# Optimization experiments

Hardware: AMD Instinct MI355X
Metric: run time of the kernel (lower is better)

## Reference

```python
import jax, jax.numpy as jnp
import numpy as np

CHUNK = 400
L = 50          # encoder kernel and stride
JUMP = CHUNK // L  # 8 new frames per streaming step
N = 128         # encoder feature dim
B = 128         # bottleneck dim
H = 512         # TCN hidden dim
K = 3           # depthwise kernel size
R, X = 2, 7     # repeats x blocks, dilations 2^0..2^6
BUF = 516       # ring buffer length: JUMP + 2*sum(dilations)*R = 8 + 508
EPS = 1e-8


def setup_inputs() -> dict:
    key = jax.random.key(0)
    ks = jax.random.split(key, 16)
    nb = R * X
    w = lambda i, shape: jax.random.normal(ks[i], shape, jnp.float32) * 0.05
    return dict(
        mixture=jax.random.normal(ks[0], (1, 2, CHUNK), jnp.float32),
        encoder_buffer=jax.random.uniform(ks[1], (1, N, BUF), dtype=jnp.float32),
        layernorm_buffer=jax.random.normal(ks[2], (1, B, BUF), jnp.float32),
        W_enc=w(3, (N, 2, L)),              # encoder Conv1d(2->N, k=L, s=L)
        ln_g=jnp.ones((N,), jnp.float32),    # channelwise LayerNorm affine
        ln_b=jnp.zeros((N,), jnp.float32),
        W_bn=w(4, (B, N)),                   # bottleneck 1x1 conv
        blk_w1=w(5, (nb, H, B)),             # per-block pointwise in
        blk_p1=jnp.full((nb,), 0.25, jnp.float32),
        blk_g1=jnp.ones((nb, H), jnp.float32),
        blk_b1=jnp.zeros((nb, H), jnp.float32),
        blk_dw=w(6, (nb, H, K)),             # depthwise dilated conv
        blk_p2=jnp.full((nb,), 0.25, jnp.float32),
        blk_g2=jnp.ones((nb, H), jnp.float32),
        blk_b2=jnp.zeros((nb, H), jnp.float32),
        blk_w2=w(7, (nb, B, H)),             # per-block pointwise out
        W_mask=w(8, (N, B)),                 # mask 1x1 conv (C=1 source)
        W_dec=w(9, (L, N)),                  # decoder basis Linear(N->L)
    )


def _cln(x, g, b):
    # channelwise LayerNorm: normalize over channel dim per time frame. x: [1,C,T]
    mu = jnp.mean(x, axis=1, keepdims=True)
    var = jnp.var(x, axis=1, keepdims=True)
    return g[None, :, None] * (x - mu) * jax.lax.rsqrt(var + EPS) + b[None, :, None]


def _prelu(x, a):
    return jnp.where(x >= 0, x, a * x)


def _dwconv(x, w, d):
    # valid dilated depthwise conv. x: [1,H,T], w: [H,K] -> [1,H,T-(K-1)*d]
    return jax.lax.conv_general_dilated(
        x, w[:, None, :], window_strides=(1,), padding='VALID',
        rhs_dilation=(d,), feature_group_count=H,
        dimension_numbers=('NCH', 'OIH', 'NCH'))


def reference(mixture, encoder_buffer, layernorm_buffer, W_enc, ln_g, ln_b, W_bn,
              blk_w1, blk_p1, blk_g1, blk_b1, blk_dw, blk_p2, blk_g2, blk_b2,
              blk_w2, W_mask, W_dec):
    # --- encoder: Conv1d(2->N, k=L, s=L) + ReLU -> JUMP new frames, ring-shift buffer
    enc = jax.nn.relu(jax.lax.conv_general_dilated(
        mixture, W_enc, window_strides=(L,), padding='VALID',
        dimension_numbers=('NCH', 'OIH', 'NCH')))          # [1,N,JUMP]
    encoder_buffer = jnp.concatenate([encoder_buffer[:, :, JUMP:], enc], axis=2)

    # --- separator front-end (network[0:2]): cLN + bottleneck 1x1, per-frame causal
    ln_new = jnp.einsum('oc,bct->bot', W_bn, _cln(enc, ln_g, ln_b))  # [1,B,JUMP]
    layernorm_buffer = jnp.concatenate([layernorm_buffer[:, :, JUMP:], ln_new], axis=2)

    # --- TCN (network[2]): valid causal dilated blocks, each shrinks time by 2*d
    x = layernorm_buffer                                   # [1,B,516]
    for i in range(R * X):
        d = 2 ** (i % X)
        y = jnp.einsum('hc,bct->bht', blk_w1[i], x)
        y = _cln(_prelu(y, blk_p1[i]), blk_g1[i], blk_b1[i])
        y = _dwconv(y, blk_dw[i], d)                       # time -= (K-1)*d
        y = _cln(_prelu(y, blk_p2[i]), blk_g2[i], blk_b2[i])
        y = jnp.einsum('ch,bht->bct', blk_w2[i], y)
        x = x[:, :, (K - 1) * d:] + y                      # residual on trailing frames
    # x: [1,B,JUMP]

    # --- mask conv (network[3]) + ReLU, reshape to [1,C=1,N,JUMP]
    mask = jax.nn.relu(jnp.einsum('nc,bct->bnt', W_mask, x)).reshape(1, 1, N, JUMP)

    # --- decoder: mask the newest JUMP encoder frames, basis Linear(N->L), stride=L
    src_w = encoder_buffer[:, None, :, -JUMP:] * mask      # [1,1,N,JUMP]
    est_source = jnp.einsum('ln,bcnt->bctl', W_dec, src_w).reshape(1, 1, JUMP * L)
    return est_source, encoder_buffer, layernorm_buffer
```

## Files before the change

### kernel.cpp

```cpp
#include <hip/hip_runtime.h>

#define CHUNK 400
#define LWIN 50
#define JUMP 8
#define NCH 128
#define BCH 128
#define HCH 512
#define NBLK 14
#define BUF 516
#define SHIFT 508
#define EPSV 1e-8f
#define NWG 136
#define NGRP 8
#define GSIZE 17

__device__ __forceinline__ void cstore(float* p, float v) {
    __hip_atomic_store(p, v, __ATOMIC_RELAXED, __HIP_MEMORY_SCOPE_AGENT);
}

__device__ __forceinline__ void gsync(unsigned* bar, int slot, int tid, int wg, int doInv) {
    __syncthreads();
    if (tid == 0) {
        unsigned* base = bar + slot * (9 * 32);
        unsigned* loc  = base + (wg & 7) * 32;
        unsigned* root = base + 8 * 32;
        unsigned prev = __hip_atomic_fetch_add(loc, 1u, __ATOMIC_RELAXED,
                                               __HIP_MEMORY_SCOPE_AGENT);
        if (prev == GSIZE - 1)
            __hip_atomic_fetch_add(root, 1u, __ATOMIC_RELAXED,
                                   __HIP_MEMORY_SCOPE_AGENT);
        while (__hip_atomic_load(root, __ATOMIC_RELAXED, __HIP_MEMORY_SCOPE_AGENT) < NGRP)
            __builtin_amdgcn_s_sleep(2);
        if (doInv)
            (void)__hip_atomic_load(root, __ATOMIC_ACQUIRE, __HIP_MEMORY_SCOPE_AGENT);
    }
    __syncthreads();
}

__device__ __forceinline__ void stage1_core(
    int tid, int lane, int wid, int t0, int nf,
    const float* __restrict__ w1b, float aPr,
    const float* __restrict__ gv, const float* __restrict__ bv,
    float* __restrict__ yout, float* redf, float* statsf, const float* xsv)
{
    float acc[4] = {0.f, 0.f, 0.f, 0.f};
    const float4* __restrict__ wr = (const float4*)(w1b + (size_t)tid * BCH);
    const float4* __restrict__ xv = (const float4*)xsv;
    #pragma unroll 4
    for (int c4 = 0; c4 < 32; ++c4) {
        float4 w = wr[c4];
        #pragma unroll
        for (int f = 0; f < 4; ++f) {
            float4 x = xv[f * 32 + c4];
            acc[f] += w.x * x.x + w.y * x.y + w.z * x.z + w.w * x.w;
        }
    }
    #pragma unroll
    for (int f = 0; f < 4; ++f) acc[f] = acc[f] >= 0.f ? acc[f] : aPr * acc[f];
    for (int f = 0; f < nf; ++f) {
        float s = acc[f], q = acc[f] * acc[f];
        #pragma unroll
        for (int o = 32; o; o >>= 1) { s += __shfl_xor(s, o); q += __shfl_xor(q, o); }
        if (lane == 0) { redf[(wid * 4 + f) * 2] = s; redf[(wid * 4 + f) * 2 + 1] = q; }
    }
    __syncthreads();
    if (tid < nf) {
        float s = 0.f, q = 0.f;
        #pragma unroll
        for (int w = 0; w < 8; ++w) { s += redf[(w * 4 + tid) * 2]; q += redf[(w * 4 + tid) * 2 + 1]; }
        float mean = s * (1.f / HCH);
        float var = q * (1.f / HCH) - mean * mean;
        statsf[tid * 2] = mean; statsf[tid * 2 + 1] = rsqrtf(var + EPSV);
    }
    __syncthreads();
    float gg = gv[tid], bb = bv[tid];
    for (int f = 0; f < nf; ++f)
        cstore(&yout[(t0 + f) * HCH + tid],
               gg * (acc[f] - statsf[f * 2]) * statsf[f * 2 + 1] + bb);
}

__global__ __launch_bounds__(512) void k_fused(
    const float* __restrict__ mixture, const float* __restrict__ inEnc,
    const float* __restrict__ inLn, const float* __restrict__ Wenc,
    const float* __restrict__ lng, const float* __restrict__ lnb,
    const float* __restrict__ Wbn, const float* __restrict__ w1,
    const float* __restrict__ p1, const float* __restrict__ g1,
    const float* __restrict__ b1, const float* __restrict__ dwc,
    const float* __restrict__ p2, const float* __restrict__ g2,
    const float* __restrict__ b2, const float* __restrict__ w2,
    const float* __restrict__ Wmask, const float* __restrict__ Wdec,
    float* __restrict__ est, float* __restrict__ outEnc, float* __restrict__ outLn,
    unsigned* __restrict__ bar, float* __restrict__ enc,
    float* __restrict__ xbuf, float* __restrict__ ybuf,
    int nx, int ny, int doInv)
{
    __shared__ float xs[4 * BCH];
    __shared__ float ys[4 * 528];
    __shared__ float redf[8 * 4 * 2];
    __shared__ float statsf[4 * 2];

    const int wg = blockIdx.x;
    const int tid = threadIdx.x;
    const int lane = tid & 63, wid = tid >> 6;

    if (wg < 8) {
        int t = wg;
        float e = 0.f;
        if (tid < 128) {
            int c = tid;
            const float* w = Wenc + c * 100;
            const float* m = mixture + t * LWIN;
            #pragma unroll 10
            for (int l = 0; l < LWIN; ++l) e += m[l] * w[l] + m[CHUNK + l] * w[LWIN + l];
            e = fmaxf(e, 0.f);
            cstore(&enc[t * NCH + c], e);
            outEnc[c * BUF + SHIFT + t] = e;
            float s = e, q = e * e;
            #pragma unroll
            for (int o = 32; o; o >>= 1) { s += __shfl_xor(s, o); q += __shfl_xor(q, o); }
            if (lane == 0) { redf[(wid * 4) * 2] = s; redf[(wid * 4) * 2 + 1] = q; }
        }
        __syncthreads();
        if (tid < 128) {
            float S = redf[0] + redf[8], Q = redf[1] + redf[9];
            float mean = S * (1.f / NCH);
            float var = Q * (1.f / NCH) - mean * mean;
            float r = rsqrtf(var + EPSV);
            xs[tid] = lng[tid] * (e - mean) * r + lnb[tid];
        }
        __syncthreads();
        if (tid < 128) {
            float acc = 0.f;
            const float4* wr = (const float4*)(Wbn + tid * NCH);
            const float4* nv = (const float4*)xs;
            #pragma unroll 8
            for (int j4 = 0; j4 < 32; ++j4) {
                float4 w = wr[j4]; float4 x = nv[j4];
                acc += w.x * x.x + w.y * x.y + w.z * x.z + w.w * x.w;
            }
            outLn[tid * BUF + SHIFT + t] = acc;
            cstore(&xbuf[(SHIFT + t) * BCH + tid], acc);
        }
    } else {
        int ch = wg - 8;
        for (int t = tid; t < SHIFT; t += 512)
            outEnc[ch * BUF + t] = inEnc[ch * BUF + t + JUMP];
        if (ch < 127) {
            int f = tid >> 7, c = tid & 127;
            int t = 4 * ch + f;
            float v = inLn[c * BUF + t + JUMP];
            cstore(&xbuf[t * BCH + c], v);
            outLn[c * BUF + t] = v;
        }
    }
    gsync(bar, 0, tid, wg, doInv);

    {
        int t0 = 4 * wg;
        if (t0 < BUF) {
            int nf = min(4, BUF - t0);
            for (int idx = tid; idx < nf * BCH; idx += 512) xs[idx] = xbuf[t0 * BCH + idx];
            __syncthreads();
            stage1_core(tid, lane, wid, t0, nf, w1, p1[0], g1, b1, ybuf, redf, statsf, xs);
        }
    }
    gsync(bar, 1, tid, wg, doInv);

    const float* xin = xbuf;
    int T = BUF;
    for (int i = 0; i < NBLK; ++i) {
        float* xout = xbuf + (size_t)((i + 1) % nx) * (BUF * BCH);
        const float* ycur = ybuf + (size_t)(i % ny) * (BUF * HCH);
        float* ynext = ybuf + (size_t)((i + 1) % ny) * (BUF * HCH);
        int d = 1 << (i % 7);
        int Tout = T - 2 * d;
        int t0 = 4 * wg;
        if (t0 < Tout) {
            int nf = min(4, Tout - t0);
            const float* dwb = dwc + (size_t)i * HCH * 3;
            float d0 = dwb[tid * 3], d1 = dwb[tid * 3 + 1], d2 = dwb[tid * 3 + 2];
            float a2 = p2[i];
            float y[4];
            for (int f = 0; f < nf; ++f) {
                int t = t0 + f;
                float v = d0 * ycur[t * HCH + tid] + d1 * ycur[(t + d) * HCH + tid]
                        + d2 * ycur[(t + 2 * d) * HCH + tid];
                y[f] = v >= 0.f ? v : a2 * v;
            }
            for (int f = 0; f < nf; ++f) {
                float s = y[f], q = y[f] * y[f];
                #pragma unroll
                for (int o = 32; o; o >>= 1) { s += __shfl_xor(s, o); q += __shfl_xor(q, o); }
                if (lane == 0) { redf[(wid * 4 + f) * 2] = s; redf[(wid * 4 + f) * 2 + 1] = q; }
            }
            __syncthreads();
            if (tid < nf) {
                float s = 0.f, q = 0.f;
                #pragma unroll
                for (int w = 0; w < 8; ++w) { s += redf[(w * 4 + tid) * 2]; q += redf[(w * 4 + tid) * 2 + 1]; }
                float mean = s * (1.f / HCH);
                float var = q * (1.f / HCH) - mean * mean;
                statsf[tid * 2] = mean; statsf[tid * 2 + 1] = rsqrtf(var + EPSV);
            }
            __syncthreads();
            {
                float gg = g2[i * HCH + tid], bb = b2[i * HCH + tid];
                int pidx = (tid >> 7) * 132 + (tid & 127);
                for (int f = 0; f < nf; ++f)
                    ys[f * 528 + pidx] = gg * (y[f] - statsf[f * 2]) * statsf[f * 2 + 1] + bb;
            }
            __syncthreads();
            int c = tid >> 2, p = tid & 3;
            float acc[4] = {0.f, 0.f, 0.f, 0.f};
            const float4* wr = (const float4*)(w2 + (size_t)i * BCH * HCH + c * HCH + p * 128);
            const float* yb = ys + p * 132;
            #pragma unroll 4
            for (int j4 = 0; j4 < 32; ++j4) {
                float4 w = wr[j4];
                #pragma unroll
                for (int f = 0; f < 4; ++f) {
                    float4 x = *(const float4*)&yb[f * 528 + j4 * 4];
                    acc[f] += w.x * x.x + w.y * x.y + w.z * x.z + w.w * x.w;
                }
            }
            for (int f = 0; f < nf; ++f) {
                acc[f] += __shfl_xor(acc[f], 1);
                acc[f] += __shfl_xor(acc[f], 2);
            }
            if (p == 0) {
                for (int f = 0; f < nf; ++f) {
                    int t = t0 + f;
                    float xv = xin[(t + 2 * d) * BCH + c] + acc[f];
                    cstore(&xout[t * BCH + c], xv);
                    xs[f * BCH + c] = xv;
                }
            }
            __syncthreads();
            if (i < NBLK - 1) {
                stage1_core(tid, lane, wid, t0, nf,
                            w1 + (size_t)(i + 1) * HCH * BCH, p1[i + 1],
                            g1 + (i + 1) * HCH, b1 + (i + 1) * HCH, ynext, redf, statsf, xs);
            } else {
                int cc = tid & 127, f = tid >> 7;
                float m = 0.f;
                const float4* wm = (const float4*)(Wmask + cc * BCH);
                const float4* xv = (const float4*)(xs + f * BCH);
                #pragma unroll 8
                for (int j4 = 0; j4 < 32; ++j4) {
                    float4 w = wm[j4]; float4 x = xv[j4];
                    m += w.x * x.x + w.y * x.y + w.z * x.z + w.w * x.w;
                }
                m = fmaxf(m, 0.f);
                ys[f * BCH + cc] = m * enc[(t0 + f) * NCH + cc];
                __syncthreads();
                if (tid < 4 * LWIN) {
                    int ff = tid / LWIN, l = tid % LWIN;
                    float e = 0.f;
                    const float4* wd = (const float4*)(Wdec + l * NCH);
                    const float4* sv = (const float4*)(ys + ff * BCH);
                    #pragma unroll 8
                    for (int j4 = 0; j4 < 32; ++j4) {
                        float4 w = wd[j4]; float4 x = sv[j4];
                        e += w.x * x.x + w.y * x.y + w.z * x.z + w.w * x.w;
                    }
                    est[(t0 + ff) * LWIN + l] = e;
                }
            }
        }
        if (i < NBLK - 1) gsync(bar, 2 + i, tid, wg, doInv);
        T = Tout;
        xin = xout;
    }
}

extern "C" void kernel_launch(void* const* d_in, const int* in_sizes, int n_in,
                              void* d_out, int out_size, void* d_ws, size_t ws_size,
                              hipStream_t stream) {
    const float* mixture = (const float*)d_in[0];
    const float* inEnc   = (const float*)d_in[1];
    const float* inLn    = (const float*)d_in[2];
    const float* Wenc    = (const float*)d_in[3];
    const float* lng     = (const float*)d_in[4];
    const float* lnb     = (const float*)d_in[5];
    const float* Wbn     = (const float*)d_in[6];
    const float* w1      = (const float*)d_in[7];
    const float* p1      = (const float*)d_in[8];
    const float* g1      = (const float*)d_in[9];
    const float* b1      = (const float*)d_in[10];
    const float* dwc     = (const float*)d_in[11];
    const float* p2      = (const float*)d_in[12];
    const float* g2      = (const float*)d_in[13];
    const float* b2      = (const float*)d_in[14];
    const float* w2      = (const float*)d_in[15];
    const float* Wmask   = (const float*)d_in[16];
    const float* Wdec    = (const float*)d_in[17];

    float* est    = (float*)d_out;
    float* outEnc = est + CHUNK;
    float* outLn  = outEnc + NCH * BUF;

    unsigned* bar = (unsigned*)d_ws;
    float* enc  = (float*)d_ws + 4608;
    float* xbuf = enc + 1024;
    const size_t xstr = (size_t)BUF * BCH;
    const size_t ystr = (size_t)BUF * HCH;
    const size_t head = 4608 + 1024;

    int nx, ny, doInv;
    size_t need_fresh = (head + 15 * xstr + 14 * ystr) * 4ull;
    if (ws_size >= need_fresh) { nx = 15; ny = 14; doInv = 0; }
    else                       { nx = 2;  ny = 2;  doInv = 1; }
    float* ybuf = xbuf + (size_t)nx * xstr;

    hipMemsetAsync(d_ws, 0, 18432, stream);

    void* args[] = { &mixture, &inEnc, &inLn, &Wenc, &lng, &lnb, &Wbn, &w1, &p1,
                     &g1, &b1, &dwc, &p2, &g2, &b2, &w2, &Wmask, &Wdec,
                     &est, &outEnc, &outLn, &bar, &enc, &xbuf, &ybuf,
                     &nx, &ny, &doInv };
    hipLaunchCooperativeKernel((const void*)k_fused, dim3(NWG), dim3(512),
                               (void**)args, 0, stream);
}
```

Baseline: 389.3 us.

## Replace grid-wide barriers with per-workgroup dataflow flags between TCN stages

Result: faster. 377.8 us (-3.0%).

```diff
diff --git a/kernel.cpp b/kernel.cpp
--- a/kernel.cpp
+++ b/kernel.cpp
@@ -18,7 +18,7 @@
     __hip_atomic_store(p, v, __ATOMIC_RELAXED, __HIP_MEMORY_SCOPE_AGENT);
 }
 
-__device__ __forceinline__ void gsync(unsigned* bar, int slot, int tid, int wg, int doInv) {
+__device__ __forceinline__ void gsync(unsigned* bar, int slot, int tid, int wg) {
     __syncthreads();
     if (tid == 0) {
         unsigned* base = bar + slot * (9 * 32);
@@ -31,10 +31,23 @@
                                    __HIP_MEMORY_SCOPE_AGENT);
         while (__hip_atomic_load(root, __ATOMIC_RELAXED, __HIP_MEMORY_SCOPE_AGENT) < NGRP)
             __builtin_amdgcn_s_sleep(2);
-        if (doInv)
-            (void)__hip_atomic_load(root, __ATOMIC_ACQUIRE, __HIP_MEMORY_SCOPE_AGENT);
-    }
-    __syncthreads();
+        (void)__hip_atomic_load(root, __ATOMIC_ACQUIRE, __HIP_MEMORY_SCOPE_AGENT);
+    }
+    __syncthreads();
+}
+
+__device__ __forceinline__ void fwait(unsigned* flp, int base, int cnt, int tid) {
+    if (tid < cnt) {
+        unsigned* p = flp + base + tid;
+        while (__hip_atomic_load(p, __ATOMIC_RELAXED, __HIP_MEMORY_SCOPE_AGENT) == 0)
+            __builtin_amdgcn_s_sleep(1);
+    }
+    __syncthreads();
+}
+__device__ __forceinline__ void fset(unsigned* flp, int idx, int tid) {
+    __syncthreads();
+    if (tid == 0)
+        __hip_atomic_store(flp + idx, 1u, __ATOMIC_RELAXED, __HIP_MEMORY_SCOPE_AGENT);
 }
 
 __device__ __forceinline__ void stage1_core(
@@ -90,9 +103,9 @@
     const float* __restrict__ b2, const float* __restrict__ w2,
     const float* __restrict__ Wmask, const float* __restrict__ Wdec,
     float* __restrict__ est, float* __restrict__ outEnc, float* __restrict__ outLn,
-    unsigned* __restrict__ bar, float* __restrict__ enc,
+    unsigned* __restrict__ fl, float* __restrict__ enc,
     float* __restrict__ xbuf, float* __restrict__ ybuf,
-    int nx, int ny, int doInv)
+    int nx, int ny, int mode)
 {
     __shared__ float xs[4 * BCH];
     __shared__ float ys[4 * 528];
@@ -102,6 +115,7 @@
     const int wg = blockIdx.x;
     const int tid = threadIdx.x;
     const int lane = tid & 63, wid = tid >> 6;
+    const int j = wg;
 
     if (wg < 8) {
         int t = wg;
@@ -153,18 +167,23 @@
             outLn[c * BUF + t] = v;
         }
     }
-    gsync(bar, 0, tid, wg, doInv);
-
-    {
-        int t0 = 4 * wg;
-        if (t0 < BUF) {
-            int nf = min(4, BUF - t0);
-            for (int idx = tid; idx < nf * BCH; idx += 512) xs[idx] = xbuf[t0 * BCH + idx];
-            __syncthreads();
-            stage1_core(tid, lane, wid, t0, nf, w1, p1[0], g1, b1, ybuf, redf, statsf, xs);
-        }
-    }
-    gsync(bar, 1, tid, wg, doInv);
+    if (mode == 0) fset(fl, 0 * NWG + wg, tid); else gsync(fl, 0, tid, wg);
+
+    if (4 * j < BUF) {
+        if (mode == 0) {
+            int base, cnt;
+            if (j <= 126)      { base = 8 + j; cnt = 1; }
+            else if (j == 127) { base = 0;     cnt = 4; }
+            else               { base = 4;     cnt = 4; }
+            fwait(fl, base, cnt, tid);
+        }
+        int t0 = 4 * j;
+        int nf = min(4, BUF - t0);
+        for (int idx = tid; idx < nf * BCH; idx += 512) xs[idx] = xbuf[t0 * BCH + idx];
+        __syncthreads();
+        stage1_core(tid, lane, wid, t0, nf, w1, p1[0], g1, b1, ybuf, redf, statsf, xs);
+    }
+    if (mode == 0) fset(fl, 1 * NWG + wg, tid); else gsync(fl, 1, tid, wg);
 
     const float* xin = xbuf;
     int T = BUF;
@@ -174,8 +193,14 @@
         float* ynext = ybuf + (size_t)((i + 1) % ny) * (BUF * HCH);
         int d = 1 << (i % 7);
         int Tout = T - 2 * d;
-        int t0 = 4 * wg;
+        int t0 = 4 * j;
         if (t0 < Tout) {
+            if (mode == 0) {
+                int jmaxe = (T - 1) >> 2;
+                int jmax = min(j + ((3 + 2 * d) >> 2), jmaxe);
+                fwait(fl + (1 + i) * NWG, j, jmax - j + 1, tid);
+                if (i == NBLK - 1) fwait(fl, 4 * j, 4, tid);
+            }
             int nf = min(4, Tout - t0);
             const float* dwb = dwc + (size_t)i * HCH * 3;
             float d0 = dwb[tid * 3], d1 = dwb[tid * 3 + 1], d2 = dwb[tid * 3 + 2];
@@ -267,7 +292,8 @@
                 }
             }
         }
-        if (i < NBLK - 1) gsync(bar, 2 + i, tid, wg, doInv);
+        if (mode == 0) fset(fl, (2 + i) * NWG + wg, tid);
+        else if (i < NBLK - 1) gsync(fl, 2 + i, tid, wg);
         T = Tout;
         xin = xout;
     }
@@ -299,25 +325,24 @@
     float* outEnc = est + CHUNK;
     float* outLn  = outEnc + NCH * BUF;
 
-    unsigned* bar = (unsigned*)d_ws;
+    unsigned* fl = (unsigned*)d_ws;
     float* enc  = (float*)d_ws + 4608;
     float* xbuf = enc + 1024;
     const size_t xstr = (size_t)BUF * BCH;
     const size_t ystr = (size_t)BUF * HCH;
-    const size_t head = 4608 + 1024;
-
-    int nx, ny, doInv;
-    size_t need_fresh = (head + 15 * xstr + 14 * ystr) * 4ull;
-    if (ws_size >= need_fresh) { nx = 15; ny = 14; doInv = 0; }
-    else                       { nx = 2;  ny = 2;  doInv = 1; }
+
+    int nx, ny, mode;
+    size_t need_fresh = (4608 + 1024 + 15 * xstr + 14 * ystr) * 4ull;
+    if (ws_size >= need_fresh) { nx = 15; ny = 14; mode = 0; }
+    else                       { nx = 2;  ny = 2;  mode = 1; }
     float* ybuf = xbuf + (size_t)nx * xstr;
 
     hipMemsetAsync(d_ws, 0, 18432, stream);
 
     void* args[] = { &mixture, &inEnc, &inLn, &Wenc, &lng, &lnb, &Wbn, &w1, &p1,
                      &g1, &b1, &dwc, &p2, &g2, &b2, &w2, &Wmask, &Wdec,
-                     &est, &outEnc, &outLn, &bar, &enc, &xbuf, &ybuf,
-                     &nx, &ny, &doInv };
+                     &est, &outEnc, &outLn, &fl, &enc, &xbuf, &ybuf,
+                     &nx, &ny, &mode };
     hipLaunchCooperativeKernel((const void*)k_fused, dim3(NWG), dim3(512),
                                (void**)args, 0, stream);
 }
```
